# Kernel tuning notes

Hardware: AMD Instinct MI355X
Metric: run time of the kernel (lower is better)

## Reference

```python
import jax, jax.numpy as jnp
import numpy as np

PAD = 0
N_SENSE = 5

def setup_inputs() -> dict:
    key = jax.random.key(0)
    k1, k2, k3, k4, k5 = jax.random.split(key, 5)
    mb, L, S, D, V, O = 256, 200, N_SENSE, 128, 50000, 50000
    inputs = jax.random.randint(k1, (mb, L * S), 0, V, dtype=jnp.int32).astype(jnp.int64)
    length_weights = jax.random.uniform(k2, (mb, 1, 1), dtype=jnp.float32)
    word_attn_mask = jnp.zeros((mb, L), dtype=bool)
    embedding = (jax.random.normal(k3, (V, D), dtype=jnp.float32) * 0.02).at[PAD].set(0.0)
    W_out = jax.random.normal(k4, (D, O), dtype=jnp.float32) * 0.02
    b_out = jnp.zeros((O,), dtype=jnp.float32)
    w_attn = jax.random.normal(k5, (D,), dtype=jnp.float32) * 0.02
    b_attn = jnp.zeros((), dtype=jnp.float32)
    return {"inputs": inputs, "length_weights": length_weights,
            "word_attn_mask": word_attn_mask, "embedding": embedding,
            "W_out": W_out, "b_out": b_out, "w_attn": w_attn, "b_attn": b_attn}

def reference(inputs, length_weights, word_attn_mask, embedding, W_out, b_out, w_attn, b_attn):
    S = N_SENSE
    mb, LS = inputs.shape
    L = LS // S
    D = embedding.shape[1]
    lw = length_weights[:, 0, 0]                      # [mb] per-example 1/length scalar
    embeds = embedding[inputs]                        # [mb, L*S, D]
    # global mean: sum over all sense-slots, scaled by length weight / n_sense
    gmean = embeds.sum(axis=1) * lw[:, None] / S      # [mb, D]
    # sense-level attention (softmax over n_sense per word slot)
    sense_imp = jnp.einsum('bld,bd->bl', embeds, gmean).reshape(mb, L, S)
    sense_w = jax.nn.softmax(sense_imp, axis=-1)      # [mb, L, S]
    word_mean = jnp.einsum('bls,blsd->bld', sense_w, embeds.reshape(mb, L, S, D))
    # word-level attention with pad mask
    word_imp = jnp.einsum('bld,d->bl', word_mean, w_attn) + b_attn
    word_imp = jnp.where(word_attn_mask, -jnp.inf, word_imp)
    word_w = jax.nn.softmax(word_imp, axis=-1)        # [mb, L]
    context = jnp.einsum('bl,bld->bd', word_w, word_mean)  # [mb, D]
    # similarity-based sense re-weighting
    sim = jnp.einsum('bld,bd->bl', embeds, context).reshape(mb, L, S)
    attn_w = jax.nn.softmax(sim, axis=-1).reshape(mb, LS)
    attn_w = attn_w * lw[:, None]
    attn_w = jnp.where(inputs == PAD, 0.0, attn_w)
    hidden = jnp.einsum('bl,bld->bd', attn_w, embeds)  # [mb, D]
    logits = hidden @ W_out + b_out
    return jax.nn.log_softmax(logits, axis=-1)
```

## Files before the change

kernel.cpp:

```cpp
#include <hip/hip_runtime.h>
#include <hip/hip_bf16.h>
#include <stdint.h>

#define MB 256
#define LW 200
#define NS 5
#define DD 128
#define OO 50000
#define LSTOK 1000

#define NSTRIPES 782
#define EMB_BLK 391

typedef __attribute__((ext_vector_type(8))) short bf16x8;
typedef __attribute__((ext_vector_type(4))) float f32x4;
typedef __attribute__((ext_vector_type(8))) unsigned short u16x8;

__device__ inline unsigned short f2bf(float f){
  unsigned u = __float_as_uint(f);
  unsigned r = (u + 0x7fffu + ((u >> 16) & 1u)) >> 16;
  return (unsigned short)r;
}
__device__ inline float bf2f(unsigned short h){
  return __uint_as_float(((unsigned)h) << 16);
}
__device__ inline unsigned packbf(float a, float b){
  return (unsigned)f2bf(a) | ((unsigned)f2bf(b) << 16);
}
__device__ inline float lo16f(unsigned p){ return __uint_as_float(p << 16); }
__device__ inline float hi16f(unsigned p){ return __uint_as_float(p & 0xffff0000u); }
__device__ inline float wsum64(float v){
  #pragma unroll
  for (int o = 1; o < 64; o <<= 1) v += __shfl_xor(v, o, 64);
  return v;
}
__device__ inline float wmax64(float v){
  #pragma unroll
  for (int o = 1; o < 64; o <<= 1) v = fmaxf(v, __shfl_xor(v, o, 64));
  return v;
}
__device__ inline float dot8(uint4 r, float4 a, float4 b){
  return lo16f(r.x)*a.x + hi16f(r.x)*a.y + lo16f(r.y)*a.z + hi16f(r.y)*a.w
       + lo16f(r.z)*b.x + hi16f(r.z)*b.y + lo16f(r.w)*b.z + hi16f(r.w)*b.w;
}
__device__ inline void acc8(uint4 r, float4& x, float4& y){
  x.x += lo16f(r.x); x.y += hi16f(r.x); x.z += lo16f(r.y); x.w += hi16f(r.y);
  y.x += lo16f(r.z); y.y += hi16f(r.z); y.z += lo16f(r.w); y.w += hi16f(r.w);
}
__device__ inline void wacc8(uint4 r, float w, float4& x, float4& y){
  x.x += w*lo16f(r.x); x.y += w*hi16f(r.x); x.z += w*lo16f(r.y); x.w += w*hi16f(r.y);
  y.x += w*lo16f(r.z); y.y += w*hi16f(r.z); y.z += w*lo16f(r.w); y.w += w*hi16f(r.w);
}
__device__ inline float gsum16(float v){
  v += __shfl_xor(v, 1, 64);
  v += __shfl_xor(v, 2, 64);
  v += __shfl_xor(v, 4, 64);
  v += __shfl_xor(v, 8, 64);
  return v;
}
__device__ inline float xg(float v){
  v += __shfl_xor(v, 16, 64);
  v += __shfl_xor(v, 32, 64);
  return v;
}
__device__ inline int sniff_f(const unsigned* p, int l){
  unsigned v = p[2*l + 1];
  return (__ballot(v != 0u) == 0ull) ? 1 : 0;
}

__global__ __launch_bounds__(256) void k_prep(const float* __restrict__ W,
                                              const float* __restrict__ emb,
                                              unsigned short* __restrict__ Wt,
                                              unsigned* __restrict__ embB){
  int blk = blockIdx.x, t = threadIdx.x;
  if (blk < NSTRIPES){
    __shared__ float tile[64][129];
    long long n0 = (long long)blk * 64;
    int j = t & 63, kk = t >> 6;
    #pragma unroll
    for (int k = kk; k < 128; k += 4){
      float v = 0.f;
      if (n0 + j < OO) v = W[(long long)k*OO + n0 + j];
      tile[j][k] = v;
    }
    __syncthreads();
    #pragma unroll
    for (int c = t; c < 4096; c += 256){
      int row = c >> 6, dw = c & 63;
      if (n0 + row < OO){
        unsigned pr = packbf(tile[row][2*dw], tile[row][2*dw+1]);
        ((unsigned*)Wt)[(n0 + row)*64 + dw] = pr;
      }
    }
  } else {
    long long base = (long long)(blk - NSTRIPES) * 16384;
    for (int i = t; i < 4096; i += 256){
      long long idx = base + (long long)i*4;
      if (idx < (long long)OO*DD){
        float4 v = *(const float4*)(emb + idx);
        uint2 o; o.x = packbf(v.x, v.y); o.y = packbf(v.z, v.w);
        *(uint2*)(embB + (idx >> 1)) = o;
      }
    }
  }
}

__global__ __launch_bounds__(1024)
void k_attn(
    const int* __restrict__ in32, const float* __restrict__ lwp,
    const unsigned char* __restrict__ maskp, const unsigned* __restrict__ embB,
    const float* __restrict__ w_attn, const float* __restrict__ b_attn_p,
    unsigned short* __restrict__ hB)
{
  __shared__ float wm[LW*DD];
  __shared__ float red[16*DD];
  __shared__ int   idL[1024];
  __shared__ float gm[DD];
  __shared__ float cx[DD];
  __shared__ float waL[DD];
  __shared__ float wimp[LW];
  __shared__ float ww[LW];

  int b = blockIdx.x, t = threadIdx.x;
  int wv = t >> 6, l = t & 63;
  int g = l >> 4, q16 = l & 15;
  int G = wv*4 + g;
  int f = sniff_f((const unsigned*)in32, l);
  long long base = (long long)b * LSTOK;
  float lw = lwp[b];

  idL[t] = (t < LSTOK) ? in32[(base + t) << f] : 0;
  if (t < DD) waL[t] = w_attn[t];
  __syncthreads();

  {
    float4 s0v = {0,0,0,0}, s1v = {0,0,0,0};
    #pragma unroll 4
    for (int j = 0; j < 16; j++){
      int id = idL[G*16 + j];
      uint4 r = *(const uint4*)(embB + (long long)id*64 + (q16 << 2));
      acc8(r, s0v, s1v);
    }
    s0v.x = xg(s0v.x); s0v.y = xg(s0v.y); s0v.z = xg(s0v.z); s0v.w = xg(s0v.w);
    s1v.x = xg(s1v.x); s1v.y = xg(s1v.y); s1v.z = xg(s1v.z); s1v.w = xg(s1v.w);
    if (g == 0){
      *(float4*)&red[wv*DD + q16*8]     = s0v;
      *(float4*)&red[wv*DD + q16*8 + 4] = s1v;
    }
  }
  __syncthreads();
  if (t < DD){
    float s = 0.f;
    #pragma unroll
    for (int r = 0; r < 16; r++) s += red[r*DD + t];
    gm[t] = s * lw * 0.2f;
  }
  __syncthreads();

  {
    float4 g0v = *(const float4*)&gm[q16*8];
    float4 g1v = *(const float4*)&gm[q16*8+4];
    float4 wa0 = *(const float4*)&waL[q16*8];
    float4 wa1 = *(const float4*)&waL[q16*8+4];
    float b_attn = *b_attn_p;
    for (int w = G; w < LW; w += 64){
      int tb = w*NS;
      uint4 e0 = *(const uint4*)(embB + (long long)idL[tb  ]*64 + (q16<<2));
      uint4 e1 = *(const uint4*)(embB + (long long)idL[tb+1]*64 + (q16<<2));
      uint4 e2 = *(const uint4*)(embB + (long long)idL[tb+2]*64 + (q16<<2));
      uint4 e3 = *(const uint4*)(embB + (long long)idL[tb+3]*64 + (q16<<2));
      uint4 e4 = *(const uint4*)(embB + (long long)idL[tb+4]*64 + (q16<<2));
      float d0 = gsum16(dot8(e0, g0v, g1v));
      float d1 = gsum16(dot8(e1, g0v, g1v));
      float d2 = gsum16(dot8(e2, g0v, g1v));
      float d3 = gsum16(dot8(e3, g0v, g1v));
      float d4 = gsum16(dot8(e4, g0v, g1v));
      float mx = fmaxf(fmaxf(fmaxf(d0,d1), fmaxf(d2,d3)), d4);
      float x0 = __expf(d0-mx), x1 = __expf(d1-mx), x2 = __expf(d2-mx),
            x3 = __expf(d3-mx), x4 = __expf(d4-mx);
      float inv = 1.0f / (x0+x1+x2+x3+x4);
      float4 m0 = {0,0,0,0}, m1 = {0,0,0,0};
      wacc8(e0, x0*inv, m0, m1);
      wacc8(e1, x1*inv, m0, m1);
      wacc8(e2, x2*inv, m0, m1);
      wacc8(e3, x3*inv, m0, m1);
      wacc8(e4, x4*inv, m0, m1);
      *(float4*)&wm[w*DD + q16*8]     = m0;
      *(float4*)&wm[w*DD + q16*8 + 4] = m1;
      float wi = m0.x*wa0.x + m0.y*wa0.y + m0.z*wa0.z + m0.w*wa0.w
               + m1.x*wa1.x + m1.y*wa1.y + m1.z*wa1.z + m1.w*wa1.w;
      wi = gsum16(wi);
      if (q16 == 0)
        wimp[w] = maskp[(long long)b*LW + w] ? -INFINITY : (wi + b_attn);
    }
  }
  __syncthreads();

  if (wv == 0){
    float v[4]; float mx = -INFINITY;
    #pragma unroll
    for (int j = 0; j < 4; j++){
      int i = l + 64*j;
      v[j] = (i < LW) ? wimp[i] : -INFINITY;
      mx = fmaxf(mx, v[j]);
    }
    mx = wmax64(mx);
    float s = 0.f;
    #pragma unroll
    for (int j = 0; j < 4; j++){
      int i = l + 64*j;
      if (i < LW){ v[j] = __expf(v[j]-mx); s += v[j]; }
    }
    s = wsum64(s);
    float inv = 1.0f / s;
    #pragma unroll
    for (int j = 0; j < 4; j++){
      int i = l + 64*j;
      if (i < LW) ww[i] = v[j]*inv;
    }
  }
  __syncthreads();

  {
    int d = t & 127, r = t >> 7;
    float s = 0.f;
    for (int w = r; w < LW; w += 8) s += ww[w]*wm[w*DD + d];
    red[r*DD + d] = s;
  }
  __syncthreads();
  if (t < DD){
    float s = 0.f;
    #pragma unroll
    for (int r = 0; r < 8; r++) s += red[r*DD + t];
    cx[t] = s;
  }
  __syncthreads();

  {
    float4 c0v = *(const float4*)&cx[q16*8];
    float4 c1v = *(const float4*)&cx[q16*8+4];
    float4 h0a = {0,0,0,0}, h1a = {0,0,0,0};
    for (int w = G; w < LW; w += 64){
      int tb = w*NS;
      int i0 = idL[tb], i1 = idL[tb+1], i2 = idL[tb+2], i3 = idL[tb+3], i4 = idL[tb+4];
      uint4 e0 = *(const uint4*)(embB + (long long)i0*64 + (q16<<2));
      uint4 e1 = *(const uint4*)(embB + (long long)i1*64 + (q16<<2));
      uint4 e2 = *(const uint4*)(embB + (long long)i2*64 + (q16<<2));
      uint4 e3 = *(const uint4*)(embB + (long long)i3*64 + (q16<<2));
      uint4 e4 = *(const uint4*)(embB + (long long)i4*64 + (q16<<2));
      float d0 = gsum16(dot8(e0, c0v, c1v));
      float d1 = gsum16(dot8(e1, c0v, c1v));
      float d2 = gsum16(dot8(e2, c0v, c1v));
      float d3 = gsum16(dot8(e3, c0v, c1v));
      float d4 = gsum16(dot8(e4, c0v, c1v));
      float mx = fmaxf(fmaxf(fmaxf(d0,d1), fmaxf(d2,d3)), d4);
      float x0 = __expf(d0-mx), x1 = __expf(d1-mx), x2 = __expf(d2-mx),
            x3 = __expf(d3-mx), x4 = __expf(d4-mx);
      float inv = lw / (x0+x1+x2+x3+x4);
      wacc8(e0, (i0 == 0) ? 0.f : x0*inv, h0a, h1a);
      wacc8(e1, (i1 == 0) ? 0.f : x1*inv, h0a, h1a);
      wacc8(e2, (i2 == 0) ? 0.f : x2*inv, h0a, h1a);
      wacc8(e3, (i3 == 0) ? 0.f : x3*inv, h0a, h1a);
      wacc8(e4, (i4 == 0) ? 0.f : x4*inv, h0a, h1a);
    }
    h0a.x = xg(h0a.x); h0a.y = xg(h0a.y); h0a.z = xg(h0a.z); h0a.w = xg(h0a.w);
    h1a.x = xg(h1a.x); h1a.y = xg(h1a.y); h1a.z = xg(h1a.z); h1a.w = xg(h1a.w);
    if (g == 0){
      *(float4*)&red[wv*DD + q16*8]     = h0a;
      *(float4*)&red[wv*DD + q16*8 + 4] = h1a;
    }
  }
  __syncthreads();
  if (t < DD){
    float s = 0.f;
    #pragma unroll
    for (int r = 0; r < 16; r++) s += red[r*DD + t];
    hB[b*DD + t] = f2bf(s);
  }
}

#define TST 66
__global__ __launch_bounds__(256) void k_gemm(
    const unsigned short* __restrict__ Wt,
    const unsigned short* __restrict__ hB,
    const float* __restrict__ b_out,
    unsigned short* __restrict__ logits,
    float* __restrict__ stats)
{
  __shared__ unsigned short Bs[64*128];
  __shared__ unsigned short T[256*TST];
  int blk = blockIdx.x;
  long long n0 = (long long)blk * 64;
  int t = threadIdx.x;

  #pragma unroll
  for (int c = t; c < 1024; c += 256){
    int n = c >> 4;
    int bo = (c & 15) << 4;
    long long ng = n0 + n;
    uint4 v = {0u,0u,0u,0u};
    if (ng < OO) v = *(const uint4*)((const char*)Wt + ng*256 + bo);
    *(uint4*)((char*)Bs + n*256 + (bo ^ ((n & 7) << 4))) = v;
  }
  __syncthreads();

  int wv = t >> 6, l = t & 63;
  int lr = l & 15, lg = l >> 4;

  bf16x8 a[4][4];
  #pragma unroll
  for (int mt = 0; mt < 4; mt++)
    #pragma unroll
    for (int ks = 0; ks < 4; ks++)
      a[mt][ks] = *(const bf16x8*)(hB + (wv*64 + mt*16 + lr)*DD + ks*32 + lg*8);

  f32x4 acc[4][4];
  #pragma unroll
  for (int mt = 0; mt < 4; mt++)
    #pragma unroll
    for (int nt = 0; nt < 4; nt++)
      acc[mt][nt] = (f32x4){0.f,0.f,0.f,0.f};

  #pragma unroll
  for (int nt = 0; nt < 4; nt++)
    #pragma unroll
    for (int ks = 0; ks < 4; ks++){
      int n = nt*16 + lr;
      int kb = (ks*32 + lg*8) * 2;
      bf16x8 bfr = *(const bf16x8*)((const char*)Bs + n*256 + (kb ^ ((n & 7) << 4)));
      #pragma unroll
      for (int mt = 0; mt < 4; mt++)
        acc[mt][nt] = __builtin_amdgcn_mfma_f32_16x16x32_bf16(a[mt][ks], bfr, acc[mt][nt], 0, 0, 0);
    }

  float bv[4]; int nvalid[4];
  #pragma unroll
  for (int nt = 0; nt < 4; nt++){
    long long ng = n0 + nt*16 + lr;
    nvalid[nt] = (ng < OO);
    bv[nt] = nvalid[nt] ? b_out[ng] : 0.f;
  }

  #pragma unroll
  for (int mt = 0; mt < 4; mt++){
    #pragma unroll
    for (int j = 0; j < 4; j++){
      int m = wv*64 + mt*16 + lg*4 + j;
      float s = 0.f;
      #pragma unroll
      for (int nt = 0; nt < 4; nt++){
        float x = acc[mt][nt][j] + bv[nt];
        T[m*TST + nt*16 + lr] = f2bf(x);
        s += nvalid[nt] ? __expf(x) : 0.f;
      }
      #pragma unroll
      for (int o = 1; o < 16; o <<= 1) s += __shfl_xor(s, o, 64);
      if (lr == 0) stats[(long long)m*NSTRIPES + blk] = s;
    }
  }
  __syncthreads();

  int vc2 = (int)((n0 + 64 <= OO ? 64 : OO - n0) >> 1);
  int hrow = l >> 5, c2 = l & 31;
  for (int it = 0; it < 32; it++){
    int m = wv*64 + it*2 + hrow;
    if (c2 < vc2){
      unsigned pr = *(const unsigned*)((const char*)T + (m*TST + 2*c2)*2);
      *(unsigned*)((char*)logits + ((long long)m*OO + n0 + 2*c2)*2) = pr;
    }
  }
}

__global__ void k_reduce(const float* __restrict__ stats, float* __restrict__ Lrow){
  int m = blockIdx.x, l = threadIdx.x;
  float s = 0.f;
  for (int i = l; i < NSTRIPES; i += 64) s += stats[(long long)m*NSTRIPES + i];
  s = wsum64(s);
  if (l == 0) Lrow[m] = __logf(s);
}

__global__ __launch_bounds__(256) void k_finalize(
    const unsigned short* __restrict__ logits,
    const float* __restrict__ Lrow, float* __restrict__ out)
{
  long long c = (long long)blockIdx.x*256 + threadIdx.x;
  int row = (int)(c / 6250);
  float Lv = Lrow[row];
  u16x8 v = *(const u16x8*)(logits + c*8);
  float4 o0, o1;
  o0.x = bf2f(v[0]) - Lv; o0.y = bf2f(v[1]) - Lv;
  o0.z = bf2f(v[2]) - Lv; o0.w = bf2f(v[3]) - Lv;
  o1.x = bf2f(v[4]) - Lv; o1.y = bf2f(v[5]) - Lv;
  o1.z = bf2f(v[6]) - Lv; o1.w = bf2f(v[7]) - Lv;
  *(float4*)(out + c*8)     = o0;
  *(float4*)(out + c*8 + 4) = o1;
}

extern "C" void kernel_launch(void* const* d_in, const int* in_sizes, int n_in,
                              void* d_out, int out_size, void* d_ws, size_t ws_size,
                              hipStream_t stream)
{
  (void)in_sizes; (void)n_in; (void)out_size; (void)ws_size;
  const void* inputs          = d_in[0];
  const float* lw             = (const float*)d_in[1];
  const unsigned char* mask   = (const unsigned char*)d_in[2];
  const float* emb            = (const float*)d_in[3];
  const float* W              = (const float*)d_in[4];
  const float* bout           = (const float*)d_in[5];
  const float* w_attn         = (const float*)d_in[6];
  const float* b_attn         = (const float*)d_in[7];

  char* ws = (char*)d_ws;
  unsigned short* Wt   = (unsigned short*)(ws);
  unsigned* embB       = (unsigned*)(ws + 12800000);
  unsigned short* logits = (unsigned short*)(ws + 12800000);
  unsigned short* hB   = (unsigned short*)(ws + 38400000);
  float* stats         = (float*)(ws + 38465536);
  float* Lrow          = (float*)(ws + 39266304);

  const int* in32 = (const int*)inputs;

  k_prep<<<NSTRIPES + EMB_BLK, 256, 0, stream>>>(W, emb, Wt, embB);
  k_attn<<<MB, 1024, 0, stream>>>(in32, lw, mask, embB, w_attn, b_attn, hB);
  k_gemm<<<NSTRIPES, 256, 0, stream>>>(Wt, hB, bout, logits, stats);
  k_reduce<<<MB, 64, 0, stream>>>(stats, Lrow);
  k_finalize<<<6250, 256, 0, stream>>>(logits, Lrow, (float*)d_out);
}
```

Baseline: 92.99 us.

## Overlap W transpose with attention kernel and fold row reduce into finalize

Moves the W_out transpose/bf16 conversion out of the prep kernel and into extra blocks of the attention kernel, so the weight conversion can run alongside the attention work and the prep kernel only converts the embedding table. The separate per-row log-sum reduction kernel is removed. Each finalize block now recomputes the log-normaliser for the one or two rows it covers from the stripe stats. This cuts two launches' worth of serialization. The costs are redundant stats reads in every finalize block, and transpose blocks that occupy 1024-thread slots with heavy LDS use.

```diff
diff --git a/kernel.cpp b/kernel.cpp
--- a/kernel.cpp
+++ b/kernel.cpp
@@ -68,39 +68,16 @@
   return (__ballot(v != 0u) == 0ull) ? 1 : 0;
 }
 
-__global__ __launch_bounds__(256) void k_prep(const float* __restrict__ W,
-                                              const float* __restrict__ emb,
-                                              unsigned short* __restrict__ Wt,
+__global__ __launch_bounds__(256) void k_prep(const float* __restrict__ emb,
                                               unsigned* __restrict__ embB){
   int blk = blockIdx.x, t = threadIdx.x;
-  if (blk < NSTRIPES){
-    __shared__ float tile[64][129];
-    long long n0 = (long long)blk * 64;
-    int j = t & 63, kk = t >> 6;
-    #pragma unroll
-    for (int k = kk; k < 128; k += 4){
-      float v = 0.f;
-      if (n0 + j < OO) v = W[(long long)k*OO + n0 + j];
-      tile[j][k] = v;
-    }
-    __syncthreads();
-    #pragma unroll
-    for (int c = t; c < 4096; c += 256){
-      int row = c >> 6, dw = c & 63;
-      if (n0 + row < OO){
-        unsigned pr = packbf(tile[row][2*dw], tile[row][2*dw+1]);
-        ((unsigned*)Wt)[(n0 + row)*64 + dw] = pr;
-      }
-    }
-  } else {
-    long long base = (long long)(blk - NSTRIPES) * 16384;
-    for (int i = t; i < 4096; i += 256){
-      long long idx = base + (long long)i*4;
-      if (idx < (long long)OO*DD){
-        float4 v = *(const float4*)(emb + idx);
-        uint2 o; o.x = packbf(v.x, v.y); o.y = packbf(v.z, v.w);
-        *(uint2*)(embB + (idx >> 1)) = o;
-      }
+  long long base = (long long)blk * 16384;
+  for (int i = t; i < 4096; i += 256){
+    long long idx = base + (long long)i*4;
+    if (idx < (long long)OO*DD){
+      float4 v = *(const float4*)(emb + idx);
+      uint2 o; o.x = packbf(v.x, v.y); o.y = packbf(v.z, v.w);
+      *(uint2*)(embB + (idx >> 1)) = o;
     }
   }
 }
@@ -110,6 +87,7 @@
     const int* __restrict__ in32, const float* __restrict__ lwp,
     const unsigned char* __restrict__ maskp, const unsigned* __restrict__ embB,
     const float* __restrict__ w_attn, const float* __restrict__ b_attn_p,
+    const float* __restrict__ W, unsigned short* __restrict__ Wt,
     unsigned short* __restrict__ hB)
 {
   __shared__ float wm[LW*DD];
@@ -121,7 +99,32 @@
   __shared__ float wimp[LW];
   __shared__ float ww[LW];
 
-  int b = blockIdx.x, t = threadIdx.x;
+  int t = threadIdx.x;
+
+  if (blockIdx.x >= MB){
+    int blk = blockIdx.x - MB;
+    float* tile = wm;
+    long long n0 = (long long)blk * 64;
+    int j = t & 63, kk = t >> 6;
+    #pragma unroll
+    for (int k = kk; k < 128; k += 16){
+      float v = 0.f;
+      if (n0 + j < OO) v = W[(long long)k*OO + n0 + j];
+      tile[j*129 + k] = v;
+    }
+    __syncthreads();
+    #pragma unroll
+    for (int c = t; c < 4096; c += 1024){
+      int row = c >> 6, dw = c & 63;
+      if (n0 + row < OO){
+        unsigned pr = packbf(tile[row*129 + 2*dw], tile[row*129 + 2*dw+1]);
+        ((unsigned*)Wt)[(n0 + row)*64 + dw] = pr;
+      }
+    }
+    return;
+  }
+
+  int b = blockIdx.x;
   int wv = t >> 6, l = t & 63;
   int g = l >> 4, q16 = l & 15;
   int G = wv*4 + g;
@@ -371,21 +374,30 @@
   }
 }
 
-__global__ void k_reduce(const float* __restrict__ stats, float* __restrict__ Lrow){
-  int m = blockIdx.x, l = threadIdx.x;
-  float s = 0.f;
-  for (int i = l; i < NSTRIPES; i += 64) s += stats[(long long)m*NSTRIPES + i];
-  s = wsum64(s);
-  if (l == 0) Lrow[m] = __logf(s);
-}
-
 __global__ __launch_bounds__(256) void k_finalize(
     const unsigned short* __restrict__ logits,
-    const float* __restrict__ Lrow, float* __restrict__ out)
+    const float* __restrict__ stats, float* __restrict__ out)
 {
-  long long c = (long long)blockIdx.x*256 + threadIdx.x;
-  int row = (int)(c / 6250);
-  float Lv = Lrow[row];
+  __shared__ float part[4];
+  __shared__ float Ls[2];
+  int blk = blockIdx.x, t = threadIdx.x;
+  int r0 = (blk*256) / 6250;
+  int r1 = (r0 + 1 < MB) ? r0 + 1 : MB - 1;
+  int half = t >> 7, li = t & 127;
+  int row = half ? r1 : r0;
+  float s = 0.f;
+  for (int i = li; i < NSTRIPES; i += 128)
+    s += stats[(long long)row*NSTRIPES + i];
+  s = wsum64(s);
+  if ((t & 63) == 0) part[t >> 6] = s;
+  __syncthreads();
+  if (t == 0) Ls[0] = __logf(part[0] + part[1]);
+  if (t == 1) Ls[1] = __logf(part[2] + part[3]);
+  __syncthreads();
+
+  long long c = (long long)blk*256 + t;
+  int rowt = (int)(c / 6250);
+  float Lv = Ls[rowt - r0];
   u16x8 v = *(const u16x8*)(logits + c*8);
   float4 o0, o1;
   o0.x = bf2f(v[0]) - Lv; o0.y = bf2f(v[1]) - Lv;
@@ -416,13 +428,12 @@
   unsigned short* logits = (unsigned short*)(ws + 12800000);
   unsigned short* hB   = (unsigned short*)(ws + 38400000);
   float* stats         = (float*)(ws + 38465536);
-  float* Lrow          = (float*)(ws + 39266304);
 
   const int* in32 = (const int*)inputs;
 
-  k_prep<<<NSTRIPES + EMB_BLK, 256, 0, stream>>>(W, emb, Wt, embB);
-  k_attn<<<MB, 1024, 0, stream>>>(in32, lw, mask, embB, w_attn, b_attn, hB);
+  k_prep<<<EMB_BLK, 256, 0, stream>>>(emb, embB);
+  k_attn<<<MB + NSTRIPES, 1024, 0, stream>>>(in32, lw, mask, embB,
+                                             w_attn, b_attn, W, Wt, hB);
   k_gemm<<<NSTRIPES, 256, 0, stream>>>(Wt, hB, bout, logits, stats);
-  k_reduce<<<MB, 64, 0, stream>>>(stats, Lrow);
-  k_finalize<<<6250, 256, 0, stream>>>(logits, Lrow, (float*)d_out);
-}
+  k_finalize<<<6250, 256, 0, stream>>>(logits, stats, (float*)d_out);
+}
```

Result: slower. 96.87 us (+4.2%).
